# Performance work log

Hardware: AMD Instinct MI355X
Metric: run time of the kernel (lower is better)

The kernel has to match this reference:

```python
import jax, jax.numpy as jnp
import numpy as np

B, C, H, W = 8, 256, 48, 48


def setup_inputs() -> dict:
    key = jax.random.key(0)
    k1, k2, k3 = jax.random.split(key, 3)
    x = jax.random.normal(k1, (B, C, H, W), dtype=jnp.float32)
    # torch zero-inits W; we randomize (scaled) so the output is non-trivial
    W_w = jax.random.normal(k2, (C, C), dtype=jnp.float32) * 0.02
    W_b = jax.random.normal(k3, (C,), dtype=jnp.float32) * 0.02
    return {"x": x, "W_w": W_w, "W_b": W_b}


def reference(x, W_w, W_b):
    b, c, h, w = x.shape
    xf = x.reshape(b, c, h * w)                      # (b, C, N), N = H*W
    # f = theta_x @ phi_x = X^T X  -> (b, N, N)
    f = jnp.einsum('bcn,bcm->bnm', xf, xf)
    p = jax.nn.softmax(f, axis=-1)                   # (b, N, N)
    # y = p @ g_x where g_x = X^T -> (b, N, C); store as (b, C, N)
    y = jnp.einsum('bnm,bcm->bcn', p, xf).reshape(b, c, h, w)
    # 1x1 conv W + bias, then residual
    W_y = jnp.einsum('oc,bchw->bohw', W_w, y) + W_b[None, :, None, None]
    return W_y + x
```

## Files before the change

### kernel.cpp

```cpp
#include <hip/hip_runtime.h>
#include <stdint.h>

#define BATCH 8
#define CH    256
#define NN    2304
#define KVB   32

typedef __bf16 bf16x8 __attribute__((ext_vector_type(8)));
typedef float  f32x4  __attribute__((ext_vector_type(4)));
typedef unsigned short u16x8 __attribute__((ext_vector_type(8)));
typedef unsigned int   u32x4 __attribute__((ext_vector_type(4)));

static __device__ inline unsigned short f2bf(float f) {
    __bf16 h = (__bf16)f;
    return __builtin_bit_cast(unsigned short, h);
}
static __device__ inline unsigned pk2(float a, float b) {
    return (unsigned)f2bf(a) | ((unsigned)f2bf(b) << 16);
}
static __device__ inline float bf2f(unsigned short u) {
    unsigned v = (unsigned)u << 16;
    return __builtin_bit_cast(float, v);
}

#define GLOAD_LDS(gp, lp) __builtin_amdgcn_global_load_lds( \
    (const __attribute__((address_space(1))) unsigned int*)(gp), \
    (__attribute__((address_space(3))) unsigned int*)(lp), 16, 0, 0)

__global__ __launch_bounds__(256) void ktrans(
    const float* __restrict__ x, const float* __restrict__ Ww,
    unsigned short* __restrict__ Xt, unsigned short* __restrict__ Wbf)
{
    const int bid = blockIdx.x;
    const int t   = threadIdx.x;
    const int TPB = 4 * 36;
    if (bid >= BATCH * TPB) {
        const int wb = bid - BATCH * TPB;
        const int base = wb * 8192 + t;
        #pragma unroll
        for (int i = 0; i < 32; ++i)
            Wbf[base + i * 256] = f2bf(Ww[base + i * 256]);
        return;
    }
    const int b    = bid / TPB;
    const int tile = bid % TPB;
    const int c0   = (tile / 36) * 64;
    const int n0   = (tile % 36) * 64;
    __shared__ float ld[64][65];
    {
        const int row = t >> 2, seg = t & 3;
        const float* src = x + ((size_t)b * CH + c0 + row) * NN + n0 + seg * 16;
        #pragma unroll
        for (int q = 0; q < 4; ++q) {
            float4 v = *reinterpret_cast<const float4*>(src + q * 4);
            ld[row][seg * 16 + q * 4 + 0] = v.x;
            ld[row][seg * 16 + q * 4 + 1] = v.y;
            ld[row][seg * 16 + q * 4 + 2] = v.z;
            ld[row][seg * 16 + q * 4 + 3] = v.w;
        }
    }
    __syncthreads();
    {
        const int j = t >> 2, cs = t & 3;
        u16x8 v0, v1;
        #pragma unroll
        for (int k = 0; k < 8; ++k) v0[k] = f2bf(ld[cs * 16 + k][j]);
        #pragma unroll
        for (int k = 0; k < 8; ++k) v1[k] = f2bf(ld[cs * 16 + 8 + k][j]);
        unsigned short* dst = Xt + ((size_t)b * NN + n0 + j) * CH + c0 + cs * 16;
        *reinterpret_cast<u16x8*>(dst)     = v0;
        *reinterpret_cast<u16x8*>(dst + 8) = v1;
    }
}

__global__ __launch_bounds__(256) void kconv(
    const unsigned short* __restrict__ Xt,
    const unsigned short* __restrict__ Wb,
    unsigned short* __restrict__ Zc)
{
    const int bid  = blockIdx.x;
    const int b    = bid & 7;
    const int rest = bid >> 3;
    const int ot   = rest / 9;
    const int nt   = rest % 9;
    const int tid  = threadIdx.x;
    const int lane = tid & 63, w = tid >> 6;
    const int lr = lane & 15, lg = lane >> 4;
    const int ob = ot * 64;
    const int nb = nt * 256 + w * 64;

    f32x4 acc[4][4];
    f32x4 z = {0.f, 0.f, 0.f, 0.f};
    #pragma unroll
    for (int og = 0; og < 4; ++og)
        #pragma unroll
        for (int ng = 0; ng < 4; ++ng) acc[og][ng] = z;

    const unsigned short* wp = Wb + (size_t)(ob + lr) * CH + lg * 8;
    const unsigned short* xp = Xt + ((size_t)b * NN + nb + lr) * CH + lg * 8;
    #pragma unroll 1
    for (int kc = 0; kc < 8; ++kc) {
        bf16x8 af[4], bf[4];
        #pragma unroll
        for (int og = 0; og < 4; ++og)
            af[og] = *reinterpret_cast<const bf16x8*>(wp + (size_t)og * 16 * CH + kc * 32);
        #pragma unroll
        for (int ng = 0; ng < 4; ++ng)
            bf[ng] = *reinterpret_cast<const bf16x8*>(xp + (size_t)ng * 16 * CH + kc * 32);
        #pragma unroll
        for (int og = 0; og < 4; ++og)
            #pragma unroll
            for (int ng = 0; ng < 4; ++ng)
                acc[og][ng] = __builtin_amdgcn_mfma_f32_16x16x32_bf16(af[og], bf[ng], acc[og][ng], 0, 0, 0);
    }
    #pragma unroll
    for (int og = 0; og < 4; ++og)
        #pragma unroll
        for (int ng = 0; ng < 4; ++ng)
            #pragma unroll
            for (int r = 0; r < 4; ++r)
                Zc[((size_t)b * CH + ob + og * 16 + lg * 4 + r) * NN + nb + ng * 16 + lr] =
                    f2bf(acc[og][ng][r]);
}

static __device__ inline bf16x8 packP(f32x4 s0, f32x4 s1, float sd, float& lsum,
                                      int lr, int lg) {
    float p0[4], p1[4];
    #pragma unroll
    for (int r = 0; r < 4; ++r) {
        p0[r] = __expf(s0[r] - sd);
        p1[r] = __expf(s1[r] - sd);
        lsum += p0[r] + p1[r];
    }
    unsigned u0 = pk2(p0[0], p0[1]), u1 = pk2(p0[2], p0[3]);
    unsigned u2 = pk2(p1[0], p1[1]), u3 = pk2(p1[2], p1[3]);
    int s0l = lr + ((lg & 1) << 5);
    unsigned a0 = (unsigned)__shfl((int)u0, s0l),      c0 = (unsigned)__shfl((int)u2, s0l);
    unsigned a1 = (unsigned)__shfl((int)u1, s0l),      c1 = (unsigned)__shfl((int)u3, s0l);
    unsigned a2 = (unsigned)__shfl((int)u0, s0l + 16), c2 = (unsigned)__shfl((int)u2, s0l + 16);
    unsigned a3 = (unsigned)__shfl((int)u1, s0l + 16), c3 = (unsigned)__shfl((int)u3, s0l + 16);
    bool hi = (lg >= 2);
    u32x4 pw;
    pw[0] = hi ? c0 : a0;
    pw[1] = hi ? c1 : a1;
    pw[2] = hi ? c2 : a2;
    pw[3] = hi ? c3 : a3;
    return __builtin_bit_cast(bf16x8, pw);
}

__global__ __launch_bounds__(256, 2) void kattn(
    const unsigned short* __restrict__ Xt,
    const unsigned short* __restrict__ Zc,
    unsigned* __restrict__ pA32,
    float* __restrict__ pL,
    int hshift)
{
    __shared__ __attribute__((aligned(16))) unsigned char smem[32768];

    const int bid  = blockIdx.x;
    const int b    = bid & 7;
    const int r    = bid >> 3;
    const int qt   = r >> hshift;
    const int h    = r & ((1 << hshift) - 1);
    const int kvh  = NN >> hshift;
    const int nit  = kvh >> 5;
    const int tid  = threadIdx.x;
    const int lane = tid & 63;
    const int w    = tid >> 6;
    const int lr = lane & 15;
    const int lg = lane >> 4;
    const int qbase = qt * 128 + w * 32;

    const unsigned short* xtb = Xt + (size_t)b * NN * CH;
    const char* kSrc = (const char*)xtb + (size_t)h * kvh * 512;
    const char* vSrc = (const char*)(Zc + (size_t)b * CH * NN) + (size_t)h * kvh * 2;

    int koff[4], voff[4];
    #pragma unroll
    for (int i = 0; i < 4; ++i) {
        int p = w * 4096 + i * 1024 + lane * 16;
        int krow = p >> 9, kc_ = p & 511;
        koff[i] = krow * 512 + (kc_ ^ ((krow & 15) << 4));
        int o = p >> 6, vc = p & 63;
        voff[i] = o * 4608 + (vc ^ (((o >> 1) & 3) << 4));
    }

    bf16x8 qa0[8], qa1[8];
    {
        const unsigned short* qp0 = xtb + (size_t)(qbase + lr) * CH + lg * 8;
        const unsigned short* qp1 = xtb + (size_t)(qbase + 16 + lr) * CH + lg * 8;
        #pragma unroll
        for (int kc = 0; kc < 8; ++kc) {
            qa0[kc] = *reinterpret_cast<const bf16x8*>(qp0 + kc * 32);
            qa1[kc] = *reinterpret_cast<const bf16x8*>(qp1 + kc * 32);
        }
    }
    float sd0 = 0.f, sd1 = 0.f;
    #pragma unroll
    for (int kc = 0; kc < 8; ++kc)
        #pragma unroll
        for (int j = 0; j < 8; ++j) {
            float v0 = (float)qa0[kc][j];
            float v1 = (float)qa1[kc][j];
            sd0 = fmaf(v0, v0, sd0);
            sd1 = fmaf(v1, v1, sd1);
        }
    sd0 += __shfl_xor(sd0, 16); sd0 += __shfl_xor(sd0, 32);
    sd1 += __shfl_xor(sd1, 16); sd1 += __shfl_xor(sd1, 32);

    f32x4 acc0[16], acc1[16];
    f32x4 zz = {0.f, 0.f, 0.f, 0.f};
    #pragma unroll
    for (int og = 0; og < 16; ++og) { acc0[og] = zz; acc1[og] = zz; }
    float ls0 = 0.f, ls1 = 0.f;

    const int kx = lr << 4;
    const int vx = (lg * 16) ^ (((lr >> 1) & 3) << 4);

    {
        unsigned char* kb = &smem[w * 4096];
        unsigned char* vb = &smem[16384 + w * 4096];
        #pragma unroll
        for (int i = 0; i < 4; ++i) GLOAD_LDS(kSrc + koff[i], kb + i * 1024);
        #pragma unroll
        for (int i = 0; i < 4; ++i) GLOAD_LDS(vSrc + voff[i], vb + i * 1024);
    }
    __syncthreads();

    #pragma unroll 1
    for (int ti = 0; ti < nit; ++ti) {
        const unsigned char* kbuf = smem;
        const unsigned char* vbuf = smem + 16384;

        f32x4 s00 = zz, s01 = zz, s10 = zz, s11 = zz;
        #pragma unroll
        for (int kc = 0; kc < 8; ++kc) {
            bf16x8 k0 = *reinterpret_cast<const bf16x8*>(kbuf + lr * 512        + ((lg * 16 + kc * 64) ^ kx));
            bf16x8 k1 = *reinterpret_cast<const bf16x8*>(kbuf + lr * 512 + 8192 + ((lg * 16 + kc * 64) ^ kx));
            s00 = __builtin_amdgcn_mfma_f32_16x16x32_bf16(k0, qa0[kc], s00, 0, 0, 0);
            s01 = __builtin_amdgcn_mfma_f32_16x16x32_bf16(k1, qa0[kc], s01, 0, 0, 0);
            s10 = __builtin_amdgcn_mfma_f32_16x16x32_bf16(k0, qa1[kc], s10, 0, 0, 0);
            s11 = __builtin_amdgcn_mfma_f32_16x16x32_bf16(k1, qa1[kc], s11, 0, 0, 0);
        }

        bf16x8 pb0 = packP(s00, s01, sd0, ls0, lr, lg);
        bf16x8 pb1 = packP(s10, s11, sd1, ls1, lr, lg);

        #pragma unroll
        for (int og = 0; og < 16; ++og) {
            bf16x8 vb = *reinterpret_cast<const bf16x8*>(vbuf + (og * 16 + lr) * 64 + vx);
            acc0[og] = __builtin_amdgcn_mfma_f32_16x16x32_bf16(vb, pb0, acc0[og], 0, 0, 0);
            acc1[og] = __builtin_amdgcn_mfma_f32_16x16x32_bf16(vb, pb1, acc1[og], 0, 0, 0);
        }

        __syncthreads();
        if (ti + 1 < nit) {
            const char* ks = kSrc + (size_t)(ti + 1) * KVB * 512;
            const char* vs = vSrc + (size_t)(ti + 1) * KVB * 2;
            unsigned char* kb = &smem[w * 4096];
            unsigned char* vb = &smem[16384 + w * 4096];
            #pragma unroll
            for (int i = 0; i < 4; ++i) GLOAD_LDS(ks + koff[i], kb + i * 1024);
            #pragma unroll
            for (int i = 0; i < 4; ++i) GLOAD_LDS(vs + voff[i], vb + i * 1024);
        }
        __syncthreads();
    }

    ls0 += __shfl_xor(ls0, 16); ls0 += __shfl_xor(ls0, 32);
    ls1 += __shfl_xor(ls1, 16); ls1 += __shfl_xor(ls1, 32);

    if (lg == 0) {
        pL[(size_t)(h * 8 + b) * NN + qbase + lr]      = ls0;
        pL[(size_t)(h * 8 + b) * NN + qbase + 16 + lr] = ls1;
    }
    const size_t rowbase = (size_t)(h * 8 + b) * 256;
    const int ub = (qbase >> 1) + lr;
    #pragma unroll
    for (int og = 0; og < 16; ++og) {
        #pragma unroll
        for (int rr = 0; rr < 4; ++rr) {
            const int o = og * 16 + lg * 4 + rr;
            pA32[(rowbase + o) * (NN / 2) + ub] = pk2(acc0[og][rr], acc1[og][rr]);
        }
    }
}

__global__ __launch_bounds__(256) void kmerge(
    const unsigned* __restrict__ pA32, const float* __restrict__ pL,
    const float* __restrict__ x, const float* __restrict__ bias,
    float* __restrict__ out, int nsplit)
{
    const int b = blockIdx.x >> 8;
    const int o = blockIdx.x & 255;
    const float bo = bias[o];
    const size_t xb = ((size_t)b * 256 + o) * NN;
    #pragma unroll
    for (int k = 0; k < 9; ++k) {
        const int n = k * 256 + threadIdx.x;
        const int ui = (n >> 5) * 16 + (n & 15);
        const int hi = (n >> 4) & 1;
        float v = 0.f, l = 0.f;
        for (int c = 0; c < nsplit; ++c) {
            unsigned pv = pA32[(((size_t)(c * 8 + b)) * 256 + o) * (NN / 2) + ui];
            v += bf2f((unsigned short)(hi ? (pv >> 16) : (pv & 0xffff)));
            l += pL[((size_t)(c * 8 + b)) * NN + n];
        }
        out[xb + n] = v / l + bo + x[xb + n];
    }
}

extern "C" void kernel_launch(void* const* d_in, const int* in_sizes, int n_in,
                              void* d_out, int out_size, void* d_ws, size_t ws_size,
                              hipStream_t stream) {
    const float* x    = (const float*)d_in[0];
    const float* Ww   = (const float*)d_in[1];
    const float* bias = (const float*)d_in[2];
    float* out = (float*)d_out;

    unsigned short* Xt  = (unsigned short*)d_ws;
    unsigned short* Zc  = Xt + (size_t)BATCH * NN * CH;
    unsigned short* Wbf = Zc + (size_t)BATCH * NN * CH;
    unsigned*       pA32 = (unsigned*)(Wbf + (size_t)CH * CH);

    const size_t base = (size_t)9437184 * 2 + 131072;
    const size_t perSplit = (size_t)BATCH * CH * NN * 2
                          + (size_t)BATCH * NN * 4;
    int hshift;
    if      (ws_size >= base + 8 * perSplit) hshift = 3;
    else if (ws_size >= base + 4 * perSplit) hshift = 2;
    else                                     hshift = 1;
    const int nsplit = 1 << hshift;
    float* pL = (float*)(pA32 + (size_t)nsplit * BATCH * CH * (NN / 2));

    ktrans<<<8 * 144 + 8,       256, 0, stream>>>(x, Ww, Xt, Wbf);
    kconv <<<288,               256, 0, stream>>>(Xt, Wbf, Zc);
    kattn <<<8 * 18 * nsplit,   256, 0, stream>>>(Xt, Zc, pA32, pL, hshift);
    kmerge<<<2048,              256, 0, stream>>>(pA32, pL, x, bias, out, nsplit);
}
```

Baseline: 129.2 us.

## Double-buffer K/V LDS tiles, add MFMA priority hints, cap KV split at four

The attention kernel now uses two 32KB LDS buffers and ping-pongs between them, issuing the global-to-LDS load for the next KV tile before computing on the current one. This takes the load latency off the critical path, where before it sat between two barriers. MFMA sections are wrapped in s_setprio hints, and sched barriers keep the prefetch ahead of the compute. The KV split is capped at 4 instead of 8, which gives fewer blocks with longer loops and less partial-result traffic for the merge. The cost is 64KB of LDS per block, which may limit occupancy to the launch-bounds target of 2 blocks per CU, and less parallelism at the lower split count.

```diff
diff --git a/kernel.cpp b/kernel.cpp
--- a/kernel.cpp
+++ b/kernel.cpp
@@ -155,7 +155,8 @@
     float* __restrict__ pL,
     int hshift)
 {
-    __shared__ __attribute__((aligned(16))) unsigned char smem[32768];
+    __shared__ __attribute__((aligned(16))) unsigned char smA[32768];
+    __shared__ __attribute__((aligned(16))) unsigned char smB[32768];
 
     const int bid  = blockIdx.x;
     const int b    = bid & 7;
@@ -217,55 +218,60 @@
     const int kx = lr << 4;
     const int vx = (lg * 16) ^ (((lr >> 1) & 3) << 4);
 
-    {
-        unsigned char* kb = &smem[w * 4096];
-        unsigned char* vb = &smem[16384 + w * 4096];
-        #pragma unroll
-        for (int i = 0; i < 4; ++i) GLOAD_LDS(kSrc + koff[i], kb + i * 1024);
-        #pragma unroll
-        for (int i = 0; i < 4; ++i) GLOAD_LDS(vSrc + voff[i], vb + i * 1024);
-    }
+    #define STAGE(sm, ti) do {                                              \
+        const char* ks_ = kSrc + (size_t)(ti) * KVB * 512;                  \
+        const char* vs_ = vSrc + (size_t)(ti) * KVB * 2;                    \
+        unsigned char* kb_ = &(sm)[w * 4096];                               \
+        unsigned char* vb_ = &(sm)[16384 + w * 4096];                       \
+        _Pragma("unroll")                                                   \
+        for (int i = 0; i < 4; ++i) GLOAD_LDS(ks_ + koff[i], kb_ + i * 1024); \
+        _Pragma("unroll")                                                   \
+        for (int i = 0; i < 4; ++i) GLOAD_LDS(vs_ + voff[i], vb_ + i * 1024); \
+    } while (0)
+
+    #define COMPUTE(sm) do {                                                \
+        const unsigned char* kbuf = (sm);                                   \
+        const unsigned char* vbuf = (sm) + 16384;                           \
+        f32x4 s00 = zz, s01 = zz, s10 = zz, s11 = zz;                       \
+        __builtin_amdgcn_s_setprio(1);                                      \
+        _Pragma("unroll")                                                   \
+        for (int kc = 0; kc < 8; ++kc) {                                    \
+            bf16x8 k0 = *reinterpret_cast<const bf16x8*>(kbuf + lr * 512        + ((lg * 16 + kc * 64) ^ kx)); \
+            bf16x8 k1 = *reinterpret_cast<const bf16x8*>(kbuf + lr * 512 + 8192 + ((lg * 16 + kc * 64) ^ kx)); \
+            s00 = __builtin_amdgcn_mfma_f32_16x16x32_bf16(k0, qa0[kc], s00, 0, 0, 0); \
+            s01 = __builtin_amdgcn_mfma_f32_16x16x32_bf16(k1, qa0[kc], s01, 0, 0, 0); \
+            s10 = __builtin_amdgcn_mfma_f32_16x16x32_bf16(k0, qa1[kc], s10, 0, 0, 0); \
+            s11 = __builtin_amdgcn_mfma_f32_16x16x32_bf16(k1, qa1[kc], s11, 0, 0, 0); \
+        }                                                                   \
+        __builtin_amdgcn_s_setprio(0);                                      \
+        bf16x8 pb0 = packP(s00, s01, sd0, ls0, lr, lg);                     \
+        bf16x8 pb1 = packP(s10, s11, sd1, ls1, lr, lg);                     \
+        __builtin_amdgcn_s_setprio(1);                                      \
+        _Pragma("unroll")                                                   \
+        for (int og = 0; og < 16; ++og) {                                   \
+            bf16x8 vb = *reinterpret_cast<const bf16x8*>(vbuf + (og * 16 + lr) * 64 + vx); \
+            acc0[og] = __builtin_amdgcn_mfma_f32_16x16x32_bf16(vb, pb0, acc0[og], 0, 0, 0); \
+            acc1[og] = __builtin_amdgcn_mfma_f32_16x16x32_bf16(vb, pb1, acc1[og], 0, 0, 0); \
+        }                                                                   \
+        __builtin_amdgcn_s_setprio(0);                                      \
+    } while (0)
+
+    STAGE(smA, 0);
     __syncthreads();
 
     #pragma unroll 1
-    for (int ti = 0; ti < nit; ++ti) {
-        const unsigned char* kbuf = smem;
-        const unsigned char* vbuf = smem + 16384;
-
-        f32x4 s00 = zz, s01 = zz, s10 = zz, s11 = zz;
-        #pragma unroll
-        for (int kc = 0; kc < 8; ++kc) {
-            bf16x8 k0 = *reinterpret_cast<const bf16x8*>(kbuf + lr * 512        + ((lg * 16 + kc * 64) ^ kx));
-            bf16x8 k1 = *reinterpret_cast<const bf16x8*>(kbuf + lr * 512 + 8192 + ((lg * 16 + kc * 64) ^ kx));
-            s00 = __builtin_amdgcn_mfma_f32_16x16x32_bf16(k0, qa0[kc], s00, 0, 0, 0);
-            s01 = __builtin_amdgcn_mfma_f32_16x16x32_bf16(k1, qa0[kc], s01, 0, 0, 0);
-            s10 = __builtin_amdgcn_mfma_f32_16x16x32_bf16(k0, qa1[kc], s10, 0, 0, 0);
-            s11 = __builtin_amdgcn_mfma_f32_16x16x32_bf16(k1, qa1[kc], s11, 0, 0, 0);
-        }
-
-        bf16x8 pb0 = packP(s00, s01, sd0, ls0, lr, lg);
-        bf16x8 pb1 = packP(s10, s11, sd1, ls1, lr, lg);
-
-        #pragma unroll
-        for (int og = 0; og < 16; ++og) {
-            bf16x8 vb = *reinterpret_cast<const bf16x8*>(vbuf + (og * 16 + lr) * 64 + vx);
-            acc0[og] = __builtin_amdgcn_mfma_f32_16x16x32_bf16(vb, pb0, acc0[og], 0, 0, 0);
-            acc1[og] = __builtin_amdgcn_mfma_f32_16x16x32_bf16(vb, pb1, acc1[og], 0, 0, 0);
-        }
-
+    for (int tp = 0; tp < nit; tp += 2) {
+        if (tp + 1 < nit) STAGE(smB, tp + 1);
+        __builtin_amdgcn_sched_barrier(0);
+        COMPUTE(smA);
         __syncthreads();
-        if (ti + 1 < nit) {
-            const char* ks = kSrc + (size_t)(ti + 1) * KVB * 512;
-            const char* vs = vSrc + (size_t)(ti + 1) * KVB * 2;
-            unsigned char* kb = &smem[w * 4096];
-            unsigned char* vb = &smem[16384 + w * 4096];
-            #pragma unroll
-            for (int i = 0; i < 4; ++i) GLOAD_LDS(ks + koff[i], kb + i * 1024);
-            #pragma unroll
-            for (int i = 0; i < 4; ++i) GLOAD_LDS(vs + voff[i], vb + i * 1024);
-        }
+        if (tp + 2 < nit) STAGE(smA, tp + 2);
+        __builtin_amdgcn_sched_barrier(0);
+        if (tp + 1 < nit) COMPUTE(smB);
         __syncthreads();
     }
+    #undef STAGE
+    #undef COMPUTE
 
     ls0 += __shfl_xor(ls0, 16); ls0 += __shfl_xor(ls0, 32);
     ls1 += __shfl_xor(ls1, 16); ls1 += __shfl_xor(ls1, 32);
@@ -327,9 +333,8 @@
     const size_t perSplit = (size_t)BATCH * CH * NN * 2
                           + (size_t)BATCH * NN * 4;
     int hshift;
-    if      (ws_size >= base + 8 * perSplit) hshift = 3;
-    else if (ws_size >= base + 4 * perSplit) hshift = 2;
-    else                                     hshift = 1;
+    if (ws_size >= base + 4 * perSplit) hshift = 2;
+    else                                hshift = 1;
     const int nsplit = 1 << hshift;
     float* pL = (float*)(pA32 + (size_t)nsplit * BATCH * CH * (NN / 2));
 
```

Measured after the change: 155.9 us. +20.6%, slower.
